# Kernel optimization log

Hardware: AMD Instinct MI355X
Metric: run time of the kernel (lower is better)

## Reference

```python
import jax, jax.numpy as jnp
import numpy as np

HEADS = 8
EPS = 1e-5


def dwconv(x, w):
    # x: [B, C, L], w: [C, 1, K] depthwise kernel (groups == C), 'same' padding (K odd)
    K = w.shape[-1]
    p = (K - 1) // 2
    return jax.lax.conv_general_dilated(
        x, w, window_strides=(1,), padding=[(p, p)],
        dimension_numbers=('NCH', 'OIH', 'NCH'),
        feature_group_count=x.shape[1])


def dds_conv(x, pw, dw3, dw15, gate):
    # DynamicDepthSeparableConv1d: 1x1 pointwise (no bias) -> two depthwise convs
    # combined with softmax-gated weighted sum.
    o = jnp.einsum('oc,bcl->bol', pw, x)
    g = jax.nn.softmax(gate)
    return g[0] * dwconv(o, dw3) + g[1] * dwconv(o, dw15)


def instance_norm(x, gamma, beta):
    # InstanceNorm1d(affine=True), biased variance over length dim
    m = jnp.mean(x, axis=-1, keepdims=True)
    v = jnp.mean((x - m) ** 2, axis=-1, keepdims=True)
    return (x - m) * jax.lax.rsqrt(v + EPS) * gamma[None, :, None] + beta[None, :, None]


def block(x, p):
    B, C, L = x.shape
    h = HEADS
    Q = dds_conv(x, p['pw_q'], p['dw3_q'], p['dw15_q'], p['gate_q']).reshape(B, h, C, L)
    K = dds_conv(x, p['pw_k'], p['dw3_k'], p['dw15_k'], p['gate_k']).reshape(B, h, C, L)
    V = dds_conv(x, p['pw_v'], p['dw3_v'], p['dw15_v'], p['gate_v']).reshape(B, h, C, L)
    scale = C ** -0.25
    # dot[b,h,k,q] = sum_c K[b,h,c,k] * Q[b,h,c,q]; softmax over key dim (axis=2)
    dot = jnp.einsum('bhck,bhcq->bhkq', K * scale, Q * scale)
    attn = jax.nn.softmax(dot, axis=2)
    o = jnp.einsum('bhck,bhkq->bhcq', V, attn).reshape(B, h * C, L)
    attended = jnp.einsum('oc,bcl->bol', p['uni_W'], o) + p['uni_b'][None, :, None]
    # dropout is identity at inference
    x = instance_norm(attended + x, p['n1_g'], p['n1_b'])
    h1 = jax.nn.relu(jnp.einsum('oc,bcl->bol', p['ffn_W1'], x) + p['ffn_b1'][None, :, None])
    ff = jnp.einsum('oc,bcl->bol', p['ffn_W2'], h1) + p['ffn_b2'][None, :, None]
    x = instance_norm(ff + x, p['n2_g'], p['n2_b'])
    return x


def setup_inputs() -> dict:
    key = jax.random.key(0)
    ks = jax.random.split(key, 32)
    D, C, h, L, B, IN = 6, 32, HEADS, 2048, 8, 6
    CH = C * h
    s = 0.05
    inp = {
        'x': jax.random.normal(ks[0], (B, IN, L), jnp.float32),
        'enc_W': jax.random.normal(ks[1], (C, IN), jnp.float32) * s,
        'enc_b': jnp.zeros((C,), jnp.float32),
        'pw_q': jax.random.normal(ks[2], (D, CH, C), jnp.float32) * s,
        'dw3_q': jax.random.normal(ks[3], (D, CH, 1, 3), jnp.float32) * s,
        'dw15_q': jax.random.normal(ks[4], (D, CH, 1, 15), jnp.float32) * s,
        'gate_q': jnp.ones((D, 2), jnp.float32),
        'pw_k': jax.random.normal(ks[5], (D, CH, C), jnp.float32) * s,
        'dw3_k': jax.random.normal(ks[6], (D, CH, 1, 3), jnp.float32) * s,
        'dw15_k': jax.random.normal(ks[7], (D, CH, 1, 15), jnp.float32) * s,
        'gate_k': jnp.ones((D, 2), jnp.float32),
        'pw_v': jax.random.normal(ks[8], (D, CH, C), jnp.float32) * s,
        'dw3_v': jax.random.normal(ks[9], (D, CH, 1, 3), jnp.float32) * s,
        'dw15_v': jax.random.normal(ks[10], (D, CH, 1, 15), jnp.float32) * s,
        'gate_v': jnp.ones((D, 2), jnp.float32),
        'uni_W': jax.random.normal(ks[11], (D, C, CH), jnp.float32) * s,
        'uni_b': jnp.zeros((D, C), jnp.float32),
        'n1_g': jnp.ones((D, C), jnp.float32),
        'n1_b': jnp.zeros((D, C), jnp.float32),
        'n2_g': jnp.ones((D, C), jnp.float32),
        'n2_b': jnp.zeros((D, C), jnp.float32),
        'ffn_W1': jax.random.normal(ks[12], (D, 4 * C, C), jnp.float32) * s,
        'ffn_b1': jnp.zeros((D, 4 * C), jnp.float32),
        'ffn_W2': jax.random.normal(ks[13], (D, C, 4 * C), jnp.float32) * s,
        'ffn_b2': jnp.zeros((D, C), jnp.float32),
        'cls_W': jax.random.normal(ks[14], (1, C), jnp.float32) * s,
        'cls_b': jnp.zeros((1,), jnp.float32),
    }
    return inp


def reference(x, enc_W, enc_b, pw_q, dw3_q, dw15_q, gate_q, pw_k, dw3_k, dw15_k,
              gate_k, pw_v, dw3_v, dw15_v, gate_v, uni_W, uni_b, n1_g, n1_b,
              n2_g, n2_b, ffn_W1, ffn_b1, ffn_W2, ffn_b2, cls_W, cls_b):
    h = jnp.einsum('oc,bcl->bol', enc_W, x) + enc_b[None, :, None]
    params = dict(pw_q=pw_q, dw3_q=dw3_q, dw15_q=dw15_q, gate_q=gate_q,
                  pw_k=pw_k, dw3_k=dw3_k, dw15_k=dw15_k, gate_k=gate_k,
                  pw_v=pw_v, dw3_v=dw3_v, dw15_v=dw15_v, gate_v=gate_v,
                  uni_W=uni_W, uni_b=uni_b, n1_g=n1_g, n1_b=n1_b,
                  n2_g=n2_g, n2_b=n2_b, ffn_W1=ffn_W1, ffn_b1=ffn_b1,
                  ffn_W2=ffn_W2, ffn_b2=ffn_b2)
    def step(carry, p):
        return block(carry, p), None
    h, _ = jax.lax.scan(step, h, params)
    logits = jnp.einsum('oc,bcl->bol', cls_W, h) + cls_b[None, :, None]  # [B,1,L]
    return jax.nn.sigmoid(logits)[:, 0, :]  # strong (per-timestep) probabilities [B, L]
```

## Files before the change

### kernel.cpp

```cpp
#include <hip/hip_runtime.h>
#include <math.h>

#define LL   2048
#define BB   8
#define CC   32
#define CHH  256
#define HH   8
#define DD   6

typedef _Float16 h8 __attribute__((ext_vector_type(8)));
typedef _Float16 h4 __attribute__((ext_vector_type(4)));
typedef float f4 __attribute__((ext_vector_type(4)));
typedef float f2v __attribute__((ext_vector_type(2)));

__global__ __launch_bounds__(256) void k_enc(const float* __restrict__ x,
    const float* __restrict__ W, const float* __restrict__ bias,
    float* __restrict__ X) {
  int idx = blockIdx.x * 256 + threadIdx.x;
  int l = idx & (LL - 1);
  int c = (idx >> 11) & 31;
  int b = idx >> 16;
  float s = bias[c];
#pragma unroll
  for (int i = 0; i < 6; ++i)
    s = fmaf(W[c * 6 + i], x[((size_t)b * 6 + i) * LL + l], s);
  X[idx] = s;
}

__global__ __launch_bounds__(256) void k_qkv(const float* __restrict__ X,
    const float* __restrict__ pwq, const float* __restrict__ pwk,
    const float* __restrict__ pwv,
    const float* __restrict__ d3q, const float* __restrict__ d15q, const float* __restrict__ gq,
    const float* __restrict__ d3k, const float* __restrict__ d15k, const float* __restrict__ gk,
    const float* __restrict__ d3v, const float* __restrict__ d15v, const float* __restrict__ gv,
    _Float16* __restrict__ Qt, _Float16* __restrict__ Kt, _Float16* __restrict__ Vt) {
  __shared__ __align__(16) char lds[21504];
  int z  = blockIdx.y;
  int bx = blockIdx.x;
  int bh = bx >> 4, lt = bx & 15, l0 = lt * 128;
  int b = bh >> 3, h = bh & 7;
  int t = threadIdx.x;
  const float* pwp  = (z == 0) ? pwq  : (z == 1) ? pwk  : pwv;
  const float* w3p  = (z == 0) ? d3q  : (z == 1) ? d3k  : d3v;
  const float* w15p = (z == 0) ? d15q : (z == 1) ? d15k : d15v;
  const float* gp   = (z == 0) ? gq   : (z == 1) ? gk   : gv;

  char* Xh = lds;
  char* Wh = lds + 9728;
  char* ot = lds + 11776;

  {
    int r = t >> 3, u = t & 7;
    const float* xr = X + ((size_t)b * CC + r) * LL;
    char* xd = Xh + r * 304;
#pragma unroll
    for (int s = u; s < 36; s += 8) {
      int ls = l0 - 8 + s * 4;
      f4 v;
      if (ls >= 0 && ls + 3 < LL) {
        v = *(const f4*)(xr + ls);
      } else {
#pragma unroll
        for (int e = 0; e < 4; ++e) {
          int l = ls + e;
          v[e] = (l >= 0 && l < LL) ? xr[l] : 0.f;
        }
      }
      uint2 pk;
      pk.x = __builtin_bit_cast(unsigned, __builtin_amdgcn_cvt_pkrtz(v[0], v[1]));
      pk.y = __builtin_bit_cast(unsigned, __builtin_amdgcn_cvt_pkrtz(v[2], v[3]));
      *(uint2*)(xd + s * 8) = pk;
    }
  }
  {
    f4 wg = ((const f4*)(pwp + h * 1024))[t];
    uint2 pk;
    pk.x = __builtin_bit_cast(unsigned, __builtin_amdgcn_cvt_pkrtz(wg[0], wg[1]));
    pk.y = __builtin_bit_cast(unsigned, __builtin_amdgcn_cvt_pkrtz(wg[2], wg[3]));
    *(uint2*)(Wh + (t >> 3) * 64 + (t & 7) * 8) = pk;
  }
  __syncthreads();

  {
    int w4 = t >> 6, lane = t & 63;
    int g = lane >> 4, ln = lane & 15;
    h8 af[2];
#pragma unroll
    for (int mt = 0; mt < 2; ++mt)
      af[mt] = *(const h8*)(Wh + (mt * 16 + ln) * 64 + g * 16);
    for (int nt = w4; nt < 9; nt += 4) {
      h8 bf;
#pragma unroll
      for (int j = 0; j < 8; ++j)
        bf[j] = *(const _Float16*)(Xh + (g * 8 + j) * 304 + (nt * 16 + ln) * 2);
#pragma unroll
      for (int mt = 0; mt < 2; ++mt) {
        f4 zr = {0.f, 0.f, 0.f, 0.f};
        f4 d = __builtin_amdgcn_mfma_f32_16x16x32_f16(af[mt], bf, zr, 0, 0, 0);
#pragma unroll
        for (int i = 0; i < 4; ++i)
          *(_Float16*)(ot + (mt * 16 + g * 4 + i) * 304 + (nt * 16 + ln) * 2) =
              (_Float16)d[i];
      }
    }
  }
  __syncthreads();

  int c = t & 31, cg = t >> 5;
  float wv[32];
  {
    const h8* wp = (const h8*)(ot + c * 304 + cg * 32);
#pragma unroll
    for (int q4 = 0; q4 < 4; ++q4) {
      h8 v = wp[q4];
#pragma unroll
      for (int e = 0; e < 8; ++e) wv[q4 * 8 + e] = (float)v[e];
    }
  }
  float r0 = gp[0], r1 = gp[1];
  float mx = fmaxf(r0, r1);
  float e0 = __expf(r0 - mx), e1 = __expf(r1 - mx);
  float gi = 1.f / (e0 + e1);
  float g0 = e0 * gi, g1 = e1 * gi;
  float sc = (z == 0) ? 0.2550765737f : 1.0f;
  int ch = h * 32 + c;
  float w3r[3], w15r[15];
#pragma unroll
  for (int k = 0; k < 3; ++k)  w3r[k]  = w3p[ch * 3 + k];
#pragma unroll
  for (int k = 0; k < 15; ++k) w15r[k] = w15p[ch * 15 + k];

  h8 olo, ohi;
#pragma unroll
  for (int i = 0; i < 16; ++i) {
    float a = 0.f;
#pragma unroll
    for (int k = 0; k < 3; ++k) a = fmaf(w3r[k], wv[i + 7 + k], a);
    float s15 = 0.f;
#pragma unroll
    for (int k = 0; k < 15; ++k) s15 = fmaf(w15r[k], wv[i + 1 + k], s15);
    float val = (g0 * a + g1 * s15) * sc;
    if (i < 8) olo[i] = (_Float16)val; else ohi[i - 8] = (_Float16)val;
  }

  if (z == 2) {
    _Float16* dst = Vt + ((size_t)bh * 32 + c) * LL + l0 + cg * 16;
    *(h8*)dst = olo;
    *(h8*)(dst + 8) = ohi;
  } else {
    char* tb = lds;
    __syncthreads();
#pragma unroll
    for (int i = 0; i < 16; ++i) {
      _Float16 v = (i < 8) ? olo[i] : ohi[i - 8];
      *(_Float16*)(tb + (cg * 16 + i) * 80 + c * 2) = v;
    }
    __syncthreads();
    _Float16* dst = ((z == 0) ? Qt : Kt) + ((size_t)bh * LL + l0) * 32;
    int l = t >> 1, hf = t & 1;
    uint4 a = *(uint4*)(tb + l * 80 + hf * 32);
    uint4 b2 = *(uint4*)(tb + l * 80 + hf * 32 + 16);
    *(uint4*)(dst + (size_t)l * 32 + hf * 16) = a;
    *(uint4*)(dst + (size_t)l * 32 + hf * 16 + 8) = b2;
  }
}

__global__ __launch_bounds__(512, 2) void k_attn(
    const _Float16* __restrict__ Qt, const _Float16* __restrict__ Kt,
    const _Float16* __restrict__ Vt, _Float16* __restrict__ AO) {
  __shared__ __align__(16) char lds[38912];
  const int tid  = threadIdx.x;
  const int lane = tid & 63;
  const int w    = tid >> 6;
  const int seg  = w >> 2;
  const int wq   = w & 3;
  const int g    = lane >> 4;
  const int ln   = lane & 15;
  const int h2c  = (wq >> 1) * 2;
  const int lin  = blockIdx.x + (blockIdx.y << 4);
  const int swz  = ((lin & 7) << 7) | (lin >> 3);
  const int qb   = swz & 15;
  const int bh   = swz >> 4;
  const _Float16* Qg = Qt + ((size_t)bh * LL + qb * 128) * 32;
  const _Float16* Kg = Kt + ((size_t)bh * LL + seg * 1024) * 32;
  const _Float16* Vg = Vt + (size_t)bh * 32 * LL + seg * 1024;

  h8 qf[2];
#pragma unroll
  for (int nt = 0; nt < 2; ++nt)
    qf[nt] = *(const h8*)(Qg + (size_t)(wq * 32 + nt * 16 + ln) * 32 + g * 8);

  h8 ones;
#pragma unroll
  for (int j = 0; j < 8; ++j) ones[j] = (_Float16)1.0f;

  char* kb = lds + seg * 5120;
  char* vb = lds + 20480 + seg * 4608;

  uint4 stg0, stg1;
  if ((wq & 1) == 0) {
    const uint4* gk = (const uint4*)Kg;
    stg0 = gk[h2c * 64 + lane];
    stg1 = gk[(h2c + 1) * 64 + lane];
    *(uint4*)(kb + (h2c * 16 + (lane >> 2)) * 80 + (lane & 3) * 16) = stg0;
    *(uint4*)(kb + ((h2c + 1) * 16 + (lane >> 2)) * 80 + (lane & 3) * 16) = stg1;
  } else {
    int c0 = h2c * 8 + (lane >> 3);
    stg0 = *(const uint4*)(Vg + (size_t)c0 * LL + (lane & 7) * 8);
    stg1 = *(const uint4*)(Vg + (size_t)(c0 + 8) * LL + (lane & 7) * 8);
    *(uint4*)(vb + c0 * 144 + (lane & 7) * 16) = stg0;
    *(uint4*)(vb + (c0 + 8) * 144 + (lane & 7) * 16) = stg1;
  }
  __syncthreads();

  f4 o[2][2];
#pragma unroll
  for (int ct = 0; ct < 2; ++ct)
#pragma unroll
    for (int nt = 0; nt < 2; ++nt) o[ct][nt] = (f4){0.f, 0.f, 0.f, 0.f};
  f4 sacc[2];
#pragma unroll
  for (int nt = 0; nt < 2; ++nt) sacc[nt] = (f4){0.f, 0.f, 0.f, 0.f};

  for (int it = 0; it < 16; ++it) {
    int pp = it & 1;
    char* kbc = kb + pp * 10240;
    char* vbc = vb + pp * 9216;
    if (it < 15) {
      int k0n = (it + 1) * 64;
      if ((wq & 1) == 0) {
        const uint4* gk = (const uint4*)(Kg + (size_t)k0n * 32);
        stg0 = gk[h2c * 64 + lane];
        stg1 = gk[(h2c + 1) * 64 + lane];
      } else {
        int c0 = h2c * 8 + (lane >> 3);
        stg0 = *(const uint4*)(Vg + (size_t)c0 * LL + k0n + (lane & 7) * 8);
        stg1 = *(const uint4*)(Vg + (size_t)(c0 + 8) * LL + k0n + (lane & 7) * 8);
      }
    }
#pragma unroll
    for (int chunk = 0; chunk < 2; ++chunk) {
      unsigned pa[2][2], pb[2][2];
#pragma unroll
      for (int mt2 = 0; mt2 < 2; ++mt2) {
        h8 kf = *(const h8*)(kbc + ((chunk * 2 + mt2) * 16 + ln) * 80 + g * 16);
#pragma unroll
        for (int nt = 0; nt < 2; ++nt) {
          f4 z = {0.f, 0.f, 0.f, 0.f};
          f4 s = __builtin_amdgcn_mfma_f32_16x16x32_f16(kf, qf[nt], z, 0, 0, 0);
          float p0 = __builtin_amdgcn_exp2f(s[0]);
          float p1 = __builtin_amdgcn_exp2f(s[1]);
          float p2 = __builtin_amdgcn_exp2f(s[2]);
          float p3 = __builtin_amdgcn_exp2f(s[3]);
          unsigned lo = __builtin_bit_cast(unsigned,
              __builtin_amdgcn_cvt_pkrtz(p0, p1));
          unsigned hi = __builtin_bit_cast(unsigned,
              __builtin_amdgcn_cvt_pkrtz(p2, p3));
          if (mt2 == 0) { pa[nt][0] = lo; pa[nt][1] = hi; }
          else          { pb[nt][0] = lo; pb[nt][1] = hi; }
        }
      }
      h8 vf[2];
#pragma unroll
      for (int ct = 0; ct < 2; ++ct)
        vf[ct] = *(const h8*)(vbc + (ct * 16 + ln) * 144 + chunk * 64 + g * 16);
#pragma unroll
      for (int nt = 0; nt < 2; ++nt) {
        unsigned w0 = pa[nt][0], w1 = pa[nt][1];
        unsigned w2 = pb[nt][0], w3 = pb[nt][1];
        asm("v_permlane32_swap_b32 %0, %1" : "+v"(w0), "+v"(w2));
        asm("v_permlane16_swap_b32 %0, %1" : "+v"(w0), "+v"(w2));
        asm("v_permlane32_swap_b32 %0, %1" : "+v"(w1), "+v"(w3));
        asm("v_permlane16_swap_b32 %0, %1" : "+v"(w1), "+v"(w3));
        uint4 pw4; pw4.x = w0; pw4.y = w1; pw4.z = w2; pw4.w = w3;
        h8 pf = __builtin_bit_cast(h8, pw4);
        sacc[nt] = __builtin_amdgcn_mfma_f32_16x16x32_f16(ones, pf, sacc[nt], 0, 0, 0);
        o[0][nt] = __builtin_amdgcn_mfma_f32_16x16x32_f16(vf[0], pf, o[0][nt], 0, 0, 0);
        o[1][nt] = __builtin_amdgcn_mfma_f32_16x16x32_f16(vf[1], pf, o[1][nt], 0, 0, 0);
      }
    }
    if (it < 15) {
      char* kbn = kb + (pp ^ 1) * 10240;
      char* vbn = vb + (pp ^ 1) * 9216;
      if ((wq & 1) == 0) {
        *(uint4*)(kbn + (h2c * 16 + (lane >> 2)) * 80 + (lane & 3) * 16) = stg0;
        *(uint4*)(kbn + ((h2c + 1) * 16 + (lane >> 2)) * 80 + (lane & 3) * 16) = stg1;
      } else {
        int c0 = h2c * 8 + (lane >> 3);
        *(uint4*)(vbn + c0 * 144 + (lane & 7) * 16) = stg0;
        *(uint4*)(vbn + (c0 + 8) * 144 + (lane & 7) * 16) = stg1;
      }
    }
    __syncthreads();
  }

  if (seg == 1) {
    char* eo = lds + wq * 9216 + lane * 144;
#pragma unroll
    for (int nt = 0; nt < 2; ++nt)
#pragma unroll
      for (int ct = 0; ct < 2; ++ct)
        *(f4*)(eo + (nt * 2 + ct) * 16) = o[ct][nt];
    f4 sv;
    sv[0] = sacc[0][0]; sv[1] = sacc[1][0];
    sv[2] = 0.f; sv[3] = 0.f;
    *(f4*)(eo + 64) = sv;
  }
  __syncthreads();
  if (seg == 0) {
    const char* po = lds + wq * 9216 + lane * 144;
    f4 s1v = *(const f4*)(po + 64);
    _Float16* out = AO + (size_t)bh * (32 * LL);
#pragma unroll
    for (int nt = 0; nt < 2; ++nt) {
      float inv = 1.f / (sacc[nt][0] + s1v[nt]);
      int qg = qb * 128 + wq * 32 + nt * 16 + ln;
#pragma unroll
      for (int ct = 0; ct < 2; ++ct) {
        f4 o1 = *(const f4*)(po + (nt * 2 + ct) * 16);
#pragma unroll
        for (int r = 0; r < 4; ++r)
          out[(size_t)(ct * 16 + g * 4 + r) * LL + qg] =
              (_Float16)((o[ct][nt][r] + o1[r]) * inv);
      }
    }
  }
}

__global__ __launch_bounds__(256) void k_uni_res(const _Float16* __restrict__ AO,
    const float* __restrict__ W, const float* __restrict__ bias,
    const float* __restrict__ Xin, float* __restrict__ Y) {
  __shared__ float ps[7][32 * 17];
  int t    = threadIdx.x;
  int li   = t & 31;
  int cg   = t >> 5;
  int bx   = blockIdx.x;
  int lt   = bx & 63;
  int half = (bx >> 6) & 1;
  int b    = bx >> 7;
  int l    = lt * 32 + li;
  const _Float16* ap = AO + (size_t)b * CHH * LL + cg * 32 * (size_t)LL + l;
  float acc[16];
#pragma unroll
  for (int j = 0; j < 16; ++j) acc[j] = 0.f;
  for (int cc = 0; cc < 32; cc += 4) {
    float a0 = (float)ap[(size_t)(cc + 0) * LL];
    float a1 = (float)ap[(size_t)(cc + 1) * LL];
    float a2 = (float)ap[(size_t)(cc + 2) * LL];
    float a3 = (float)ap[(size_t)(cc + 3) * LL];
#pragma unroll
    for (int j = 0; j < 16; ++j) {
      const float* wr = W + (half * 16 + j) * CHH + cg * 32 + cc;
      acc[j] = fmaf(wr[0], a0, acc[j]);
      acc[j] = fmaf(wr[1], a1, acc[j]);
      acc[j] = fmaf(wr[2], a2, acc[j]);
      acc[j] = fmaf(wr[3], a3, acc[j]);
    }
  }
  if (cg) {
#pragma unroll
    for (int j = 0; j < 16; ++j) ps[cg - 1][li * 17 + j] = acc[j];
  }
  __syncthreads();
  if (!cg) {
#pragma unroll
    for (int j = 0; j < 16; ++j) {
      int c = half * 16 + j;
      size_t o = ((size_t)b * CC + c) * LL + l;
      float r = acc[j] + bias[c] + Xin[o];
#pragma unroll
      for (int q = 0; q < 7; ++q) r += ps[q][li * 17 + j];
      Y[o] = r;
    }
  }
}

__global__ __launch_bounds__(512) void k_inorm(const float* __restrict__ Y,
    float* __restrict__ X, const float* __restrict__ g,
    const float* __restrict__ bt) {
  __shared__ float red[16];
  int row = blockIdx.x;
  int c = row & 31;
  const float* y = Y + (size_t)row * LL;
  float v[4];
  float s = 0.f, ss = 0.f;
#pragma unroll
  for (int i = 0; i < 4; ++i) {
    v[i] = y[threadIdx.x + 512 * i];
    s += v[i];
    ss = fmaf(v[i], v[i], ss);
  }
#pragma unroll
  for (int off = 32; off; off >>= 1) {
    s  += __shfl_down(s, off);
    ss += __shfl_down(ss, off);
  }
  int wid = threadIdx.x >> 6;
  if ((threadIdx.x & 63) == 0) { red[wid * 2] = s; red[wid * 2 + 1] = ss; }
  __syncthreads();
  if (threadIdx.x == 0) {
    float rs0 = 0.f, rs1 = 0.f;
#pragma unroll
    for (int i = 0; i < 8; ++i) { rs0 += red[i * 2]; rs1 += red[i * 2 + 1]; }
    red[0] = rs0; red[1] = rs1;
  }
  __syncthreads();
  float mean = red[0] * (1.f / LL);
  float var  = red[1] * (1.f / LL) - mean * mean;
  float rs = rsqrtf(var + 1e-5f) * g[c];
  float bb = bt[c];
#pragma unroll
  for (int i = 0; i < 4; ++i)
    X[(size_t)row * LL + threadIdx.x + 512 * i] = (v[i] - mean) * rs + bb;
}

__global__ __launch_bounds__(256) void k_ffn(const float* __restrict__ X,
    const float* __restrict__ W1, const float* __restrict__ b1,
    const float* __restrict__ W2, const float* __restrict__ b2,
    float* __restrict__ Y) {
  __shared__ __align__(16) float wlds[8320];
  __shared__ float ps[7][32 * 33];
  int bx = blockIdx.x;
  int b = bx >> 6;
  int l0 = (bx & 63) * 32;
  int t = threadIdx.x;
  int li = t & 31;
  int og = t >> 5;
  int l = l0 + li;
#pragma unroll
  for (int i = 0; i < 4; ++i)
    ((f4*)wlds)[t + i * 256] = ((const f4*)W1)[t + i * 256];
#pragma unroll
  for (int i = 0; i < 4; ++i)
    ((f4*)(wlds + 4096))[t + i * 256] = ((const f4*)W2)[t + i * 256];
  if (t < 32) ((f4*)(wlds + 8192))[t] = ((const f4*)b1)[t];

  const float* Xp = X + (size_t)b * CC * LL + l;
  float xv[32];
#pragma unroll
  for (int c = 0; c < 32; ++c) xv[c] = Xp[(size_t)c * LL];
  __syncthreads();

  float hs[16];
#pragma unroll
  for (int op = 0; op < 16; ++op) {
    int o = og * 16 + op;
    const f4* wr = (const f4*)(wlds + o * 32);
    f4 p = {wlds[8192 + o], 0.f, 0.f, 0.f};
#pragma unroll
    for (int c4 = 0; c4 < 8; ++c4) {
      f4 a = wr[c4];
      p[0] = fmaf(a[0], xv[c4 * 4 + 0], p[0]);
      p[1] = fmaf(a[1], xv[c4 * 4 + 1], p[1]);
      p[2] = fmaf(a[2], xv[c4 * 4 + 2], p[2]);
      p[3] = fmaf(a[3], xv[c4 * 4 + 3], p[3]);
    }
    hs[op] = fmaxf((p[0] + p[1]) + (p[2] + p[3]), 0.f);
  }

  float acc[32];
#pragma unroll
  for (int c = 0; c < 32; ++c) {
    const f4* w2r = (const f4*)(wlds + 4096 + c * 128 + og * 16);
    f4 s = {0.f, 0.f, 0.f, 0.f};
#pragma unroll
    for (int o4 = 0; o4 < 4; ++o4) {
      f4 w = w2r[o4];
      s[0] = fmaf(w[0], hs[o4 * 4 + 0], s[0]);
      s[1] = fmaf(w[1], hs[o4 * 4 + 1], s[1]);
      s[2] = fmaf(w[2], hs[o4 * 4 + 2], s[2]);
      s[3] = fmaf(w[3], hs[o4 * 4 + 3], s[3]);
    }
    acc[c] = (s[0] + s[1]) + (s[2] + s[3]);
  }

  if (og) {
#pragma unroll
    for (int c = 0; c < 32; ++c) ps[og - 1][li * 33 + c] = acc[c];
  }
  __syncthreads();
  if (!og) {
    float* Yp = Y + (size_t)b * CC * LL + l;
#pragma unroll
    for (int c = 0; c < 32; ++c) {
      float r = acc[c] + b2[c] + xv[c];
#pragma unroll
      for (int q = 0; q < 7; ++q) r += ps[q][li * 33 + c];
      Yp[(size_t)c * LL] = r;
    }
  }
}

__global__ __launch_bounds__(256) void k_cls(const float* __restrict__ X,
    const float* __restrict__ W, const float* __restrict__ bias,
    float* __restrict__ out) {
  int idx = blockIdx.x * 256 + threadIdx.x;
  int l = idx & (LL - 1);
  int b = idx >> 11;
  float s = bias[0];
#pragma unroll
  for (int c = 0; c < CC; ++c)
    s = fmaf(W[c], X[((size_t)b * CC + c) * LL + l], s);
  out[idx] = 1.f / (1.f + __expf(-s));
}

extern "C" void kernel_launch(void* const* d_in, const int* in_sizes, int n_in,
                              void* d_out, int out_size, void* d_ws,
                              size_t ws_size, hipStream_t stream) {
  const float* x      = (const float*)d_in[0];
  const float* enc_W  = (const float*)d_in[1];
  const float* enc_b  = (const float*)d_in[2];
  const float* pw_q   = (const float*)d_in[3];
  const float* dw3_q  = (const float*)d_in[4];
  const float* dw15_q = (const float*)d_in[5];
  const float* gate_q = (const float*)d_in[6];
  const float* pw_k   = (const float*)d_in[7];
  const float* dw3_k  = (const float*)d_in[8];
  const float* dw15_k = (const float*)d_in[9];
  const float* gate_k = (const float*)d_in[10];
  const float* pw_v   = (const float*)d_in[11];
  const float* dw3_v  = (const float*)d_in[12];
  const float* dw15_v = (const float*)d_in[13];
  const float* gate_v = (const float*)d_in[14];
  const float* uni_W  = (const float*)d_in[15];
  const float* uni_b  = (const float*)d_in[16];
  const float* n1_g   = (const float*)d_in[17];
  const float* n1_b   = (const float*)d_in[18];
  const float* n2_g   = (const float*)d_in[19];
  const float* n2_b   = (const float*)d_in[20];
  const float* ffn_W1 = (const float*)d_in[21];
  const float* ffn_b1 = (const float*)d_in[22];
  const float* ffn_W2 = (const float*)d_in[23];
  const float* ffn_b2 = (const float*)d_in[24];
  const float* cls_W  = (const float*)d_in[25];
  const float* cls_b  = (const float*)d_in[26];

  float* ws = (float*)d_ws;
  float* X   = ws;
  float* Y   = ws + 524288;
  _Float16* AO = (_Float16*)(ws + 1048576);
  _Float16* Qt = (_Float16*)(ws + 9437184);
  _Float16* Kt = (_Float16*)(ws + 11534336);
  _Float16* Vt = (_Float16*)(ws + 13631488);

  k_enc<<<2048, 256, 0, stream>>>(x, enc_W, enc_b, X);

  for (int d = 0; d < DD; ++d) {
    k_qkv<<<dim3(1024, 3), 256, 0, stream>>>(X,
        pw_q + d * CHH * CC, pw_k + d * CHH * CC, pw_v + d * CHH * CC,
        dw3_q + d * CHH * 3, dw15_q + d * CHH * 15, gate_q + d * 2,
        dw3_k + d * CHH * 3, dw15_k + d * CHH * 15, gate_k + d * 2,
        dw3_v + d * CHH * 3, dw15_v + d * CHH * 15, gate_v + d * 2,
        Qt, Kt, Vt);
    k_attn<<<dim3(16, 64), 512, 0, stream>>>(Qt, Kt, Vt, AO);
    k_uni_res<<<1024, 256, 0, stream>>>(AO, uni_W + d * CC * CHH,
                                        uni_b + d * CC, X, Y);
    k_inorm<<<256, 512, 0, stream>>>(Y, X, n1_g + d * CC, n1_b + d * CC);
    k_ffn<<<512, 256, 0, stream>>>(X, ffn_W1 + d * 128 * CC, ffn_b1 + d * 128,
                                   ffn_W2 + d * CC * 128, ffn_b2 + d * CC, Y);
    k_inorm<<<256, 512, 0, stream>>>(Y, X, n2_g + d * CC, n2_b + d * CC);
  }

  k_cls<<<64, 256, 0, stream>>>(X, cls_W, cls_b, (float*)d_out);
}
```

Measured before the change: 746.7 us.

## Rewrite unify-heads projection as fp16 MFMA GEMM with LDS-staged tiles

```diff
diff --git a/kernel.cpp b/kernel.cpp
--- a/kernel.cpp
+++ b/kernel.cpp
@@ -330,48 +330,49 @@
 __global__ __launch_bounds__(256) void k_uni_res(const _Float16* __restrict__ AO,
     const float* __restrict__ W, const float* __restrict__ bias,
     const float* __restrict__ Xin, float* __restrict__ Y) {
-  __shared__ float ps[7][32 * 17];
-  int t    = threadIdx.x;
-  int li   = t & 31;
-  int cg   = t >> 5;
-  int bx   = blockIdx.x;
-  int lt   = bx & 63;
-  int half = (bx >> 6) & 1;
-  int b    = bx >> 7;
-  int l    = lt * 32 + li;
-  const _Float16* ap = AO + (size_t)b * CHH * LL + cg * 32 * (size_t)LL + l;
-  float acc[16];
-#pragma unroll
-  for (int j = 0; j < 16; ++j) acc[j] = 0.f;
-  for (int cc = 0; cc < 32; cc += 4) {
-    float a0 = (float)ap[(size_t)(cc + 0) * LL];
-    float a1 = (float)ap[(size_t)(cc + 1) * LL];
-    float a2 = (float)ap[(size_t)(cc + 2) * LL];
-    float a3 = (float)ap[(size_t)(cc + 3) * LL];
-#pragma unroll
-    for (int j = 0; j < 16; ++j) {
-      const float* wr = W + (half * 16 + j) * CHH + cg * 32 + cc;
-      acc[j] = fmaf(wr[0], a0, acc[j]);
-      acc[j] = fmaf(wr[1], a1, acc[j]);
-      acc[j] = fmaf(wr[2], a2, acc[j]);
-      acc[j] = fmaf(wr[3], a3, acc[j]);
-    }
-  }
-  if (cg) {
-#pragma unroll
-    for (int j = 0; j < 16; ++j) ps[cg - 1][li * 17 + j] = acc[j];
-  }
-  __syncthreads();
-  if (!cg) {
-#pragma unroll
-    for (int j = 0; j < 16; ++j) {
-      int c = half * 16 + j;
-      size_t o = ((size_t)b * CC + c) * LL + l;
-      float r = acc[j] + bias[c] + Xin[o];
-#pragma unroll
-      for (int q = 0; q < 7; ++q) r += ps[q][li * 17 + j];
-      Y[o] = r;
-    }
+  __shared__ __align__(16) char lds[35840];
+  char* Wh = lds;
+  char* Bh = lds + 17920;
+  int t  = threadIdx.x;
+  int bx = blockIdx.x;
+  int lt = bx & 63, b = bx >> 6;
+  int l0 = lt * 32;
+
+#pragma unroll
+  for (int i = 0; i < 8; ++i) {
+    int idx = t + i * 256;
+    f4 wv4 = ((const f4*)W)[idx];
+    uint2 pk;
+    pk.x = __builtin_bit_cast(unsigned, __builtin_amdgcn_cvt_pkrtz(wv4[0], wv4[1]));
+    pk.y = __builtin_bit_cast(unsigned, __builtin_amdgcn_cvt_pkrtz(wv4[2], wv4[3]));
+    int c = idx >> 6, ccp = idx & 63;
+    *(uint2*)(Wh + c * 560 + ccp * 8) = pk;
+  }
+#pragma unroll
+  for (int it = 0; it < 4; ++it) {
+    int cc = it * 64 + (t >> 2), chunk = t & 3;
+    h8 av = *(const h8*)(AO + ((size_t)b * CHH + cc) * LL + l0 + chunk * 8);
+#pragma unroll
+    for (int e = 0; e < 8; ++e)
+      *(_Float16*)(Bh + (chunk * 8 + e) * 560 + cc * 2) = av[e];
+  }
+  __syncthreads();
+
+  int wv = t >> 6, lane = t & 63;
+  int g = lane >> 4, ln = lane & 15;
+  int mt = wv >> 1, nt2 = wv & 1;
+  f4 acc = {0.f, 0.f, 0.f, 0.f};
+#pragma unroll
+  for (int ks = 0; ks < 8; ++ks) {
+    h8 af = *(const h8*)(Wh + (mt * 16 + ln) * 560 + (ks * 32 + g * 8) * 2);
+    h8 bf = *(const h8*)(Bh + (nt2 * 16 + ln) * 560 + (ks * 32 + g * 8) * 2);
+    acc = __builtin_amdgcn_mfma_f32_16x16x32_f16(af, bf, acc, 0, 0, 0);
+  }
+#pragma unroll
+  for (int i = 0; i < 4; ++i) {
+    int c = mt * 16 + g * 4 + i;
+    size_t o = ((size_t)b * CC + c) * LL + l0 + nt2 * 16 + ln;
+    Y[o] = acc[i] + bias[c] + Xin[o];
   }
 }
 
@@ -553,8 +554,8 @@
         dw3_v + d * CHH * 3, dw15_v + d * CHH * 15, gate_v + d * 2,
         Qt, Kt, Vt);
     k_attn<<<dim3(16, 64), 512, 0, stream>>>(Qt, Kt, Vt, AO);
-    k_uni_res<<<1024, 256, 0, stream>>>(AO, uni_W + d * CC * CHH,
-                                        uni_b + d * CC, X, Y);
+    k_uni_res<<<512, 256, 0, stream>>>(AO, uni_W + d * CC * CHH,
+                                       uni_b + d * CC, X, Y);
     k_inorm<<<256, 512, 0, stream>>>(Y, X, n1_g + d * CC, n1_b + d * CC);
     k_ffn<<<512, 256, 0, stream>>>(X, ffn_W1 + d * 128 * CC, ffn_b1 + d * 128,
                                    ffn_W2 + d * CC * 128, ffn_b2 + d * CC, Y);
```

Result: faster. 663.4 us (-11.2%).
